# Kernel tuning notes

Hardware: AMD Instinct MI355X
Metric: run time of the kernel (lower is better)

Reference implementation:

```python
import jax, jax.numpy as jnp
import numpy as np

B, S, D = 2, 2048, 2048
NQ, NKV = 32, 8
HD = D // NQ  # 64
THETA = 10000.0


def _rope_tables(seq_len, head_dim, theta):
    k = jnp.arange(0, head_dim, 2)[: head_dim // 2].astype(jnp.float32)
    inv_freq = 1.0 / (theta ** (k / head_dim))
    pos = jnp.arange(seq_len, dtype=jnp.float32)
    ang = pos[:, None] * inv_freq[None, :]          # [S, HD/2]
    ang = jnp.concatenate([ang, ang], axis=-1)       # [S, HD]
    return jnp.cos(ang), jnp.sin(ang)


def _apply_rope(x, cos, sin):
    # x: [B, H, S, HD]; cos/sin: [S, HD]
    h = x.shape[-1] // 2
    x1, x2 = x[..., :h], x[..., h:]
    rotated = jnp.concatenate([-x2, x1], axis=-1)
    return (x * cos[None, None] + rotated * sin[None, None]).astype(x.dtype)


def setup_inputs() -> dict:
    key = jax.random.key(0)
    ks = jax.random.split(key, 6)
    x = jax.random.normal(ks[0], (B, S, D), dtype=jnp.float32)
    attention_mask = jnp.ones((B, S), dtype=jnp.int32)
    Wq = jax.random.normal(ks[1], (NQ * HD, D), dtype=jnp.float32) * 0.02
    Wk = jax.random.normal(ks[2], (NKV * HD, D), dtype=jnp.float32) * 0.02
    Wv = jax.random.normal(ks[3], (NKV * HD, D), dtype=jnp.float32) * 0.02
    Wo = jax.random.normal(ks[4], (D, D), dtype=jnp.float32) * 0.02
    return {"x": x, "attention_mask": attention_mask,
            "Wq": Wq, "Wk": Wk, "Wv": Wv, "Wo": Wo}


def reference(x, attention_mask, Wq, Wk, Wv, Wo):
    b, s, d = x.shape
    # projections (nn.Linear: y = x @ W.T)
    q = jnp.einsum('bsd,od->bso', x, Wq).reshape(b, s, NQ, HD).transpose(0, 2, 1, 3)
    k = jnp.einsum('bsd,od->bso', x, Wk).reshape(b, s, NKV, HD).transpose(0, 2, 1, 3)
    v = jnp.einsum('bsd,od->bso', x, Wv).reshape(b, s, NKV, HD).transpose(0, 2, 1, 3)
    cos, sin = _rope_tables(s, HD, THETA)
    q = _apply_rope(q, cos, sin)
    k = _apply_rope(k, cos, sin)
    g = NQ // NKV
    k = jnp.repeat(k, g, axis=1)  # [b, NQ, s, HD]
    v = jnp.repeat(v, g, axis=1)
    attn = jnp.einsum('bhqd,bhkd->bhqk', q, k)
    causal = jnp.triu(jnp.ones((s, s), dtype=bool), k=1)
    attn = jnp.where(causal[None, None], -jnp.inf, attn)
    attn = jax.nn.softmax(attn / jnp.sqrt(jnp.float32(HD)), axis=-1)
    out = jnp.einsum('bhqk,bhkd->bhqd', attn, v)
    out = out.transpose(0, 2, 1, 3).reshape(b, s, d)
    return jnp.einsum('bsd,od->bso', out, Wo)
```

## Files before the change

### kernel.cpp

```cpp
#include <hip/hip_runtime.h>

#define B_   2
#define S_   2048
#define D_   2048
#define NQ_  32
#define NKV_ 8
#define HD_  64

typedef unsigned short u16;
typedef __bf16 bf16x8 __attribute__((ext_vector_type(8)));
typedef __bf16 bf16x4 __attribute__((ext_vector_type(4)));
typedef short  s16x4  __attribute__((ext_vector_type(4)));
typedef float  f32x4  __attribute__((ext_vector_type(4)));

#define GLB __attribute__((address_space(1)))
#define LDS __attribute__((address_space(3)))

__device__ inline u16 f2b(float f){
  union { float f; unsigned u; } v; v.f = f;
  unsigned r = (v.u + 0x7fffu + ((v.u >> 16) & 1u)) >> 16;
  return (u16)r;
}

__device__ inline f32x4 mfma16(bf16x4 a, bf16x4 b, f32x4 c){
  union U { bf16x4 b; s16x4 s; };
  U ua, ub; ua.b = a; ub.b = b;
  return __builtin_amdgcn_mfma_f32_16x16x16bf16_1k(ua.s, ub.s, c, 0, 0, 0);
}

__global__ void k_f2b_all(const float* __restrict__ x,  const float* __restrict__ wq,
                          const float* __restrict__ wk, const float* __restrict__ wv,
                          const float* __restrict__ wo,
                          u16* __restrict__ xb, u16* __restrict__ wqkvb, u16* __restrict__ wob){
  int i = blockIdx.x * blockDim.x + threadIdx.x;
  const float* src; u16* dst; int off;
  if (i < 2097152)      { src = x;  dst = xb;                  off = i; }
  else if (i < 3145728) { src = wq; dst = wqkvb;               off = i - 2097152; }
  else if (i < 3407872) { src = wk; dst = wqkvb + 2048*2048;   off = i - 3145728; }
  else if (i < 3670016) { src = wv; dst = wqkvb + 2560*2048;   off = i - 3407872; }
  else                  { src = wo; dst = wob;                 off = i - 3670016; }
  float4 f = ((const float4*)src)[off];
  uint2 pk;
  pk.x = (unsigned)f2b(f.x) | ((unsigned)f2b(f.y) << 16);
  pk.y = (unsigned)f2b(f.z) | ((unsigned)f2b(f.w) << 16);
  ((uint2*)dst)[off] = pk;
}

#define GEMM_CORE(K)                                                           \
  __shared__ __align__(16) u16 As[128*64];                                     \
  __shared__ __align__(16) u16 Bs[128*64];                                     \
  const int tid  = threadIdx.x;                                               \
  const int lane = tid & 63;                                                  \
  const int wave = tid >> 6;                                                  \
  const int wm = wave >> 1, wn = wave & 1;                                    \
  const int quad = lane >> 4, l16 = lane & 15;                                \
  const u16* Ab = A  + (size_t)blockIdx.y * 128 * (K);                        \
  const u16* Bb = Bm + (size_t)blockIdx.x * 128 * (K);                        \
  f32x4 acc[4][4];                                                            \
  for (int i = 0; i < 4; i++)                                                 \
    for (int j = 0; j < 4; j++) acc[i][j] = (f32x4){0.f, 0.f, 0.f, 0.f};      \
  const int R0 = wave * 32;                                                   \
  const int lr = lane >> 3;                                                   \
  const int gc = ((lane & 7) ^ lr) * 8;                                       \
  const int sk = l16 & 7;                                                     \
  for (int k0 = 0; k0 < (K); k0 += 64){                                       \
    __syncthreads();                                                          \
    _Pragma("unroll")                                                         \
    for (int m = 0; m < 4; m++){                                              \
      const u16* ga = Ab + (size_t)(R0 + m*8 + lr) * (K) + k0 + gc;           \
      const u16* gb = Bb + (size_t)(R0 + m*8 + lr) * (K) + k0 + gc;           \
      __builtin_amdgcn_global_load_lds((const GLB void*)ga, (LDS void*)&As[(R0 + m*8)*64], 16, 0, 0); \
      __builtin_amdgcn_global_load_lds((const GLB void*)gb, (LDS void*)&Bs[(R0 + m*8)*64], 16, 0, 0); \
    }                                                                          \
    __syncthreads();                                                          \
    bf16x8 af[4][2], bfr[4][2];                                               \
    _Pragma("unroll")                                                         \
    for (int i = 0; i < 4; i++)                                               \
      _Pragma("unroll")                                                       \
      for (int h = 0; h < 2; h++)                                             \
        af[i][h]  = *(const bf16x8*)&As[(wm*64 + i*16 + l16)*64 + (((h*4 + quad) ^ sk)*8)]; \
    _Pragma("unroll")                                                         \
    for (int j = 0; j < 4; j++)                                               \
      _Pragma("unroll")                                                       \
      for (int h = 0; h < 2; h++)                                             \
        bfr[j][h] = *(const bf16x8*)&Bs[(wn*64 + j*16 + l16)*64 + (((h*4 + quad) ^ sk)*8)]; \
    _Pragma("unroll")                                                         \
    for (int i = 0; i < 4; i++)                                               \
      _Pragma("unroll")                                                       \
      for (int j = 0; j < 4; j++){                                            \
        acc[i][j] = __builtin_amdgcn_mfma_f32_16x16x32_bf16(af[i][0], bfr[j][0], acc[i][j], 0, 0, 0); \
        acc[i][j] = __builtin_amdgcn_mfma_f32_16x16x32_bf16(af[i][1], bfr[j][1], acc[i][j], 0, 0, 0); \
      }                                                                        \
  }

#define QSCALE 0.18033688011112042f
__global__ __launch_bounds__(256, 3) void k_gemm_qkv(const u16* __restrict__ A,
                                                     const u16* __restrict__ Bm,
                                                     u16* __restrict__ qT,
                                                     u16* __restrict__ kT,
                                                     u16* __restrict__ vT){
  GEMM_CORE(2048)

  const int cb = blockIdx.x*128 + wn*64;

  if (cb < 2560){
    const bool isq = (cb < 2048);
    const int hh   = (isq ? cb : (cb - 2048)) >> 6;
    const int NH   = isq ? NQ_ : NKV_;
    u16* base      = isq ? qT : kT;
    const float sc = isq ? QSCALE : 1.0f;
    #pragma unroll
    for (int j = 0; j < 2; j++){
      const int d2 = j*16 + l16;
      const float invf = __expf(-(float)d2 * (9.210340371976184f / 32.0f));
      #pragma unroll
      for (int i = 0; i < 4; i++){
        const int row0 = blockIdx.y*128 + wm*64 + i*16 + quad*4;
        #pragma unroll
        for (int r = 0; r < 4; r++){
          const int row = row0 + r;
          const int s = row & (S_ - 1), b = row >> 11;
          float ang = (float)s * invf;
          float sn = __sinf(ang), cs = __cosf(ang);
          const float x1 = acc[i][j][r] * sc, x2 = acc[i][j+2][r] * sc;
          u16* drow = base + ((size_t)(b*NH + hh) * S_ + s) * 64;
          drow[d2]      = f2b(x1*cs - x2*sn);
          drow[d2 + 32] = f2b(x2*cs + x1*sn);
        }
      }
    }
  } else {
    const int fbase = cb - 2560;
    #pragma unroll
    for (int j = 0; j < 4; j++){
      const int f = fbase + j*16 + l16;
      const int kvh = f >> 6, d = f & 63;
      #pragma unroll
      for (int i = 0; i < 4; i++){
        const int row0 = blockIdx.y*128 + wm*64 + i*16 + quad*4;
        const int s0 = row0 & (S_ - 1), b = row0 >> 11;
        uint2 pk;
        pk.x = (unsigned)f2b(acc[i][j][0]) | ((unsigned)f2b(acc[i][j][1]) << 16);
        pk.y = (unsigned)f2b(acc[i][j][2]) | ((unsigned)f2b(acc[i][j][3]) << 16);
        *(uint2*)(vT + ((size_t)(b*NKV_ + kvh) * 64 + d) * S_ + s0) = pk;
      }
    }
  }
}

__global__ __launch_bounds__(256, 3) void k_gemm_bt(const u16* __restrict__ A,
                                                    const u16* __restrict__ Bm,
                                                    float* __restrict__ C,
                                                    int N){
  GEMM_CORE(2048)
  for (int i = 0; i < 4; i++){
    int row0 = blockIdx.y*128 + wm*64 + i*16 + quad*4;
    for (int j = 0; j < 4; j++){
      int col = blockIdx.x*128 + wn*64 + j*16 + l16;
      for (int r = 0; r < 4; r++)
        C[(size_t)(row0 + r) * N + col] = acc[i][j][r];
    }
  }
}

__global__ __launch_bounds__(256) void k_attn(const u16* __restrict__ qT,
                                              const u16* __restrict__ kT,
                                              const u16* __restrict__ vT,
                                              u16* __restrict__ aout){
  __shared__ __align__(16) u16 Ks[2][64*64];
  __shared__ __align__(16) u16 Vs[2][64*64];

  const int bid  = blockIdx.x;
  const int tp   = bid & 7;
  const int h    = (bid >> 3) & 31;
  const int b    = bid >> 8;
  const int kvh  = h >> 2;
  const int lane = threadIdx.x & 63, w = threadIdx.x >> 6;
  const int quad = lane >> 4, l16 = lane & 15;

  const u16* Qh = qT + (size_t)(b*NQ_ + h)    * S_ * 64;
  const u16* Kh = kT + (size_t)(b*NKV_ + kvh) * S_ * 64;
  const u16* Vh = vT + (size_t)(b*NKV_ + kvh) * 64 * S_;

  const int rr = lane >> 3;
  const int gg = (lane & 7) ^ rr;
  const int R  = w * 16;

  auto stage = [&](int c, int buf){
    const int kb = c * 64;
    const u16* gk0 = Kh + (size_t)(kb + R + rr)     * 64 + gg*8;
    const u16* gk1 = Kh + (size_t)(kb + R + 8 + rr) * 64 + gg*8;
    const u16* gv0 = Vh + (size_t)(R + rr)     * S_ + kb + gg*8;
    const u16* gv1 = Vh + (size_t)(R + 8 + rr) * S_ + kb + gg*8;
    __builtin_amdgcn_global_load_lds((const GLB void*)gk0, (LDS void*)&Ks[buf][R*64],     16, 0, 0);
    __builtin_amdgcn_global_load_lds((const GLB void*)gk1, (LDS void*)&Ks[buf][(R+8)*64], 16, 0, 0);
    __builtin_amdgcn_global_load_lds((const GLB void*)gv0, (LDS void*)&Vs[buf][R*64],     16, 0, 0);
    __builtin_amdgcn_global_load_lds((const GLB void*)gv1, (LDS void*)&Vs[buf][(R+8)*64], 16, 0, 0);
  };

  const int sw = l16 & 7;

  for (int ph = 0; ph < 2; ph++){
    const int T   = ph ? (15 - tp) : tp;
    const int qb0 = 2*T, qb1 = 2*T + 1;
    const int qr0 = T*128 + w*16 + l16;
    const int qr1 = qr0 + 64;

    if (ph == 1) __syncthreads();
    stage(0, 0);

    bf16x8 qf[2][2];
    qf[0][0] = *(const bf16x8*)(Qh + (size_t)qr0*64 + quad*8);
    qf[0][1] = *(const bf16x8*)(Qh + (size_t)qr0*64 + 32 + quad*8);
    qf[1][0] = *(const bf16x8*)(Qh + (size_t)qr1*64 + quad*8);
    qf[1][1] = *(const bf16x8*)(Qh + (size_t)qr1*64 + 32 + quad*8);

    f32x4 o[2][4];
    #pragma unroll
    for (int s = 0; s < 2; s++)
      for (int dt = 0; dt < 4; dt++) o[s][dt] = (f32x4){0.f, 0.f, 0.f, 0.f};
    float lrow[2] = {0.f, 0.f};

    for (int c = 0; c <= qb1; c++){
      const int buf = c & 1;
      __syncthreads();
      if (c < qb1) stage(c+1, buf^1);

      const bool act0  = (c <= qb0);
      const bool diag0 = (c == qb0);
      const bool diag1 = (c == qb1);

      bf16x4 pk[2][4];
      #pragma unroll
      for (int t = 0; t < 4; t++){
        const bool n0 = act0 && !(diag0 && t > w);
        const bool n1 = !(diag1 && t > w);
        if (!n0 && !n1) continue;
        const int row = t*16 + l16;
        bf16x8 ka0 = *(const bf16x8*)&Ks[buf][row*64 + (((quad    ) ^ sw)*8)];
        bf16x8 ka1 = *(const bf16x8*)&Ks[buf][row*64 + (((quad + 4) ^ sw)*8)];
        #pragma unroll
        for (int s = 0; s < 2; s++){
          if (s == 0 ? !n0 : !n1) continue;
          f32x4 z = (f32x4){0.f, 0.f, 0.f, 0.f};
          z = __builtin_amdgcn_mfma_f32_16x16x32_bf16(ka0, qf[s][0], z, 0, 0, 0);
          z = __builtin_amdgcn_mfma_f32_16x16x32_bf16(ka1, qf[s][1], z, 0, 0, 0);
          if ((s == 0 ? diag0 : diag1) && t == w){
            #pragma unroll
            for (int r = 0; r < 4; r++)
              if (quad*4 + r > l16) z[r] = -1e30f;
          }
          #pragma unroll
          for (int r = 0; r < 4; r++){
            float p = exp2f(z[r]);
            lrow[s] += p;
            pk[s][t][r] = (__bf16)p;
          }
        }
      }

      #pragma unroll
      for (int dt = 0; dt < 4; dt++){
        const int row = dt*16 + l16;
        #pragma unroll
        for (int t = 0; t < 4; t++){
          const bool n0 = act0 && !(diag0 && t > w);
          const bool n1 = !(diag1 && t > w);
          if (!n0 && !n1) continue;
          const int ch = (2*t + (quad >> 1)) ^ sw;
          bf16x4 va = *(const bf16x4*)&Vs[buf][row*64 + ch*8 + (quad & 1)*4];
          if (n0) o[0][dt] = mfma16(va, pk[0][t], o[0][dt]);
          if (n1) o[1][dt] = mfma16(va, pk[1][t], o[1][dt]);
        }
      }
    }

    #pragma unroll
    for (int s = 0; s < 2; s++){
      float lsum = lrow[s];
      lsum += __shfl_xor(lsum, 16, 64);
      lsum += __shfl_xor(lsum, 32, 64);
      float inv = 1.0f / lsum;
      const int qrow = s ? qr1 : qr0;
      u16* orow = aout + (size_t)(b*S_ + qrow) * D_ + h*64;
      #pragma unroll
      for (int dt = 0; dt < 4; dt++){
        uint2 pkd;
        u16 e0 = f2b(o[s][dt][0] * inv), e1 = f2b(o[s][dt][1] * inv);
        u16 e2 = f2b(o[s][dt][2] * inv), e3 = f2b(o[s][dt][3] * inv);
        pkd.x = (unsigned)e0 | ((unsigned)e1 << 16);
        pkd.y = (unsigned)e2 | ((unsigned)e3 << 16);
        *(uint2*)(orow + dt*16 + quad*4) = pkd;
      }
    }
  }
}

extern "C" void kernel_launch(void* const* d_in, const int* in_sizes, int n_in,
                              void* d_out, int out_size, void* d_ws, size_t ws_size,
                              hipStream_t stream){
  const float* x  = (const float*)d_in[0];
  const float* Wq = (const float*)d_in[2];
  const float* Wk = (const float*)d_in[3];
  const float* Wv = (const float*)d_in[4];
  const float* Wo = (const float*)d_in[5];

  char* ws = (char*)d_ws;
  u16* xb    = (u16*)(ws);
  u16* wqkvb = (u16*)(ws + 16777216);
  u16* wob   = (u16*)(ws + 29360128);
  u16* qTp   = (u16*)(ws + 37748736);
  u16* kTp   = (u16*)(ws + 54525952);
  u16* vTp   = (u16*)(ws + 58720256);
  u16* attnOut = xb;

  k_f2b_all<<<dim3(18432), 256, 0, stream>>>(x, Wq, Wk, Wv, Wo, xb, wqkvb, wob);

  k_gemm_qkv<<<dim3(24, 32), 256, 0, stream>>>(xb, wqkvb, qTp, kTp, vTp);

  k_attn<<<dim3(512), 256, 0, stream>>>(qTp, kTp, vTp, attnOut);

  k_gemm_bt<<<dim3(16, 32), 256, 0, stream>>>(attnOut, wob, (float*)d_out, 2048);
}
```

Before: 301.4 us.

## Split attention blocks per query tile, heavy-first order, cheaper exp and bf16 pack

The attention grid goes from 512 blocks, each handling a balanced pair of query tiles (T and 15-T), to 1024 blocks that each handle one 128-row tile. Tiles are scheduled largest-first, and the index order places the 8 KV heads and both batches in adjacent blocks, which may help K/V cache locality and load balance. The inner loop also switches to the hardware exp2 builtin, packs P to bf16 by truncation instead of rounding, and hoists the swizzle offsets. Truncating P loses a little precision, and single-tile blocks redo per-block setup and Q loads.

New measurement: 297.4 us. Within noise of the previous version (-1.3%).

```diff
diff --git a/kernel.cpp b/kernel.cpp
--- a/kernel.cpp
+++ b/kernel.cpp
@@ -26,6 +26,15 @@
   union U { bf16x4 b; s16x4 s; };
   U ua, ub; ua.b = a; ub.b = b;
   return __builtin_amdgcn_mfma_f32_16x16x16bf16_1k(ua.s, ub.s, c, 0, 0, 0);
+}
+
+__device__ inline bf16x4 pack4(float p0, float p1, float p2, float p3){
+  union { float f; unsigned u; } a, b, c, d;
+  a.f = p0; b.f = p1; c.f = p2; d.f = p3;
+  union { uint2 u; bf16x4 v; } r;
+  r.u.x = (a.u >> 16) | (b.u & 0xffff0000u);
+  r.u.y = (c.u >> 16) | (d.u & 0xffff0000u);
+  return r.v;
 }
 
 __global__ void k_f2b_all(const float* __restrict__ x,  const float* __restrict__ wq,
@@ -170,11 +179,12 @@
   __shared__ __align__(16) u16 Ks[2][64*64];
   __shared__ __align__(16) u16 Vs[2][64*64];
 
-  const int bid  = blockIdx.x;
-  const int tp   = bid & 7;
-  const int h    = (bid >> 3) & 31;
-  const int b    = bid >> 8;
-  const int kvh  = h >> 2;
+  const int bid = blockIdx.x;
+  const int kvh = bid & 7;
+  const int b   = (bid >> 3) & 1;
+  const int hq  = (bid >> 4) & 3;
+  const int T   = 15 - (bid >> 6);
+  const int h   = kvh*4 + hq;
   const int lane = threadIdx.x & 63, w = threadIdx.x >> 6;
   const int quad = lane >> 4, l16 = lane & 15;
 
@@ -198,100 +208,103 @@
     __builtin_amdgcn_global_load_lds((const GLB void*)gv1, (LDS void*)&Vs[buf][(R+8)*64], 16, 0, 0);
   };
 
-  const int sw = l16 & 7;
-
-  for (int ph = 0; ph < 2; ph++){
-    const int T   = ph ? (15 - tp) : tp;
-    const int qb0 = 2*T, qb1 = 2*T + 1;
-    const int qr0 = T*128 + w*16 + l16;
-    const int qr1 = qr0 + 64;
-
-    if (ph == 1) __syncthreads();
-    stage(0, 0);
-
-    bf16x8 qf[2][2];
-    qf[0][0] = *(const bf16x8*)(Qh + (size_t)qr0*64 + quad*8);
-    qf[0][1] = *(const bf16x8*)(Qh + (size_t)qr0*64 + 32 + quad*8);
-    qf[1][0] = *(const bf16x8*)(Qh + (size_t)qr1*64 + quad*8);
-    qf[1][1] = *(const bf16x8*)(Qh + (size_t)qr1*64 + 32 + quad*8);
-
-    f32x4 o[2][4];
-    #pragma unroll
-    for (int s = 0; s < 2; s++)
-      for (int dt = 0; dt < 4; dt++) o[s][dt] = (f32x4){0.f, 0.f, 0.f, 0.f};
-    float lrow[2] = {0.f, 0.f};
-
-    for (int c = 0; c <= qb1; c++){
-      const int buf = c & 1;
-      __syncthreads();
-      if (c < qb1) stage(c+1, buf^1);
-
-      const bool act0  = (c <= qb0);
-      const bool diag0 = (c == qb0);
-      const bool diag1 = (c == qb1);
-
-      bf16x4 pk[2][4];
+  const int sw    = l16 & 7;
+  const int koff0 = ((quad    ) ^ sw) * 8;
+  const int koff1 = ((quad + 4) ^ sw) * 8;
+  int voff[4];
+  #pragma unroll
+  for (int t = 0; t < 4; t++)
+    voff[t] = (((2*t + (quad >> 1)) ^ sw) * 8) + (quad & 1)*4;
+
+  const int qb0 = 2*T, qb1 = 2*T + 1;
+  const int qr0 = T*128 + w*16 + l16;
+  const int qr1 = qr0 + 64;
+
+  stage(0, 0);
+
+  bf16x8 qf[2][2];
+  qf[0][0] = *(const bf16x8*)(Qh + (size_t)qr0*64 + quad*8);
+  qf[0][1] = *(const bf16x8*)(Qh + (size_t)qr0*64 + 32 + quad*8);
+  qf[1][0] = *(const bf16x8*)(Qh + (size_t)qr1*64 + quad*8);
+  qf[1][1] = *(const bf16x8*)(Qh + (size_t)qr1*64 + 32 + quad*8);
+
+  f32x4 o[2][4];
+  #pragma unroll
+  for (int s = 0; s < 2; s++)
+    for (int dt = 0; dt < 4; dt++) o[s][dt] = (f32x4){0.f, 0.f, 0.f, 0.f};
+  float lrow[2] = {0.f, 0.f};
+
+  for (int c = 0; c <= qb1; c++){
+    const int buf = c & 1;
+    __syncthreads();
+    if (c < qb1) stage(c+1, buf^1);
+
+    const bool act0  = (c <= qb0);
+    const bool diag0 = (c == qb0);
+    const bool diag1 = (c == qb1);
+    const u16* Kb = &Ks[buf][0];
+    const u16* Vb = &Vs[buf][0];
+
+    bf16x4 pk[2][4];
+    #pragma unroll
+    for (int t = 0; t < 4; t++){
+      const bool n0 = act0 && !(diag0 && t > w);
+      const bool n1 = !(diag1 && t > w);
+      if (!n0 && !n1) continue;
+      const int rowb = (t*16 + l16)*64;
+      bf16x8 ka0 = *(const bf16x8*)&Kb[rowb + koff0];
+      bf16x8 ka1 = *(const bf16x8*)&Kb[rowb + koff1];
+      #pragma unroll
+      for (int s = 0; s < 2; s++){
+        if (s == 0 ? !n0 : !n1) continue;
+        f32x4 z = (f32x4){0.f, 0.f, 0.f, 0.f};
+        z = __builtin_amdgcn_mfma_f32_16x16x32_bf16(ka0, qf[s][0], z, 0, 0, 0);
+        z = __builtin_amdgcn_mfma_f32_16x16x32_bf16(ka1, qf[s][1], z, 0, 0, 0);
+        if ((s == 0 ? diag0 : diag1) && t == w){
+          #pragma unroll
+          for (int r = 0; r < 4; r++)
+            if (quad*4 + r > l16) z[r] = -1e30f;
+        }
+        float p0 = __builtin_amdgcn_exp2f(z[0]);
+        float p1 = __builtin_amdgcn_exp2f(z[1]);
+        float p2 = __builtin_amdgcn_exp2f(z[2]);
+        float p3 = __builtin_amdgcn_exp2f(z[3]);
+        lrow[s] += (p0 + p1) + (p2 + p3);
+        pk[s][t] = pack4(p0, p1, p2, p3);
+      }
+    }
+
+    #pragma unroll
+    for (int dt = 0; dt < 4; dt++){
+      const int rowb = (dt*16 + l16)*64;
       #pragma unroll
       for (int t = 0; t < 4; t++){
         const bool n0 = act0 && !(diag0 && t > w);
         const bool n1 = !(diag1 && t > w);
         if (!n0 && !n1) continue;
-        const int row = t*16 + l16;
-        bf16x8 ka0 = *(const bf16x8*)&Ks[buf][row*64 + (((quad    ) ^ sw)*8)];
-        bf16x8 ka1 = *(const bf16x8*)&Ks[buf][row*64 + (((quad + 4) ^ sw)*8)];
-        #pragma unroll
-        for (int s = 0; s < 2; s++){
-          if (s == 0 ? !n0 : !n1) continue;
-          f32x4 z = (f32x4){0.f, 0.f, 0.f, 0.f};
-          z = __builtin_amdgcn_mfma_f32_16x16x32_bf16(ka0, qf[s][0], z, 0, 0, 0);
-          z = __builtin_amdgcn_mfma_f32_16x16x32_bf16(ka1, qf[s][1], z, 0, 0, 0);
-          if ((s == 0 ? diag0 : diag1) && t == w){
-            #pragma unroll
-            for (int r = 0; r < 4; r++)
-              if (quad*4 + r > l16) z[r] = -1e30f;
-          }
-          #pragma unroll
-          for (int r = 0; r < 4; r++){
-            float p = exp2f(z[r]);
-            lrow[s] += p;
-            pk[s][t][r] = (__bf16)p;
-          }
-        }
+        bf16x4 va = *(const bf16x4*)&Vb[rowb + voff[t]];
+        if (n0) o[0][dt] = mfma16(va, pk[0][t], o[0][dt]);
+        if (n1) o[1][dt] = mfma16(va, pk[1][t], o[1][dt]);
       }
-
-      #pragma unroll
-      for (int dt = 0; dt < 4; dt++){
-        const int row = dt*16 + l16;
-        #pragma unroll
-        for (int t = 0; t < 4; t++){
-          const bool n0 = act0 && !(diag0 && t > w);
-          const bool n1 = !(diag1 && t > w);
-          if (!n0 && !n1) continue;
-          const int ch = (2*t + (quad >> 1)) ^ sw;
-          bf16x4 va = *(const bf16x4*)&Vs[buf][row*64 + ch*8 + (quad & 1)*4];
-          if (n0) o[0][dt] = mfma16(va, pk[0][t], o[0][dt]);
-          if (n1) o[1][dt] = mfma16(va, pk[1][t], o[1][dt]);
-        }
-      }
-    }
-
-    #pragma unroll
-    for (int s = 0; s < 2; s++){
-      float lsum = lrow[s];
-      lsum += __shfl_xor(lsum, 16, 64);
-      lsum += __shfl_xor(lsum, 32, 64);
-      float inv = 1.0f / lsum;
-      const int qrow = s ? qr1 : qr0;
-      u16* orow = aout + (size_t)(b*S_ + qrow) * D_ + h*64;
-      #pragma unroll
-      for (int dt = 0; dt < 4; dt++){
-        uint2 pkd;
-        u16 e0 = f2b(o[s][dt][0] * inv), e1 = f2b(o[s][dt][1] * inv);
-        u16 e2 = f2b(o[s][dt][2] * inv), e3 = f2b(o[s][dt][3] * inv);
-        pkd.x = (unsigned)e0 | ((unsigned)e1 << 16);
-        pkd.y = (unsigned)e2 | ((unsigned)e3 << 16);
-        *(uint2*)(orow + dt*16 + quad*4) = pkd;
-      }
+    }
+  }
+
+  #pragma unroll
+  for (int s = 0; s < 2; s++){
+    float lsum = lrow[s];
+    lsum += __shfl_xor(lsum, 16, 64);
+    lsum += __shfl_xor(lsum, 32, 64);
+    float inv = 1.0f / lsum;
+    const int qrow = s ? qr1 : qr0;
+    u16* orow = aout + (size_t)(b*S_ + qrow) * D_ + h*64;
+    #pragma unroll
+    for (int dt = 0; dt < 4; dt++){
+      uint2 pkd;
+      u16 e0 = f2b(o[s][dt][0] * inv), e1 = f2b(o[s][dt][1] * inv);
+      u16 e2 = f2b(o[s][dt][2] * inv), e3 = f2b(o[s][dt][3] * inv);
+      pkd.x = (unsigned)e0 | ((unsigned)e1 << 16);
+      pkd.y = (unsigned)e2 | ((unsigned)e3 << 16);
+      *(uint2*)(orow + dt*16 + quad*4) = pkd;
     }
   }
 }
@@ -318,7 +331,7 @@
 
   k_gemm_qkv<<<dim3(24, 32), 256, 0, stream>>>(xb, wqkvb, qTp, kTp, vTp);
 
-  k_attn<<<dim3(512), 256, 0, stream>>>(qTp, kTp, vTp, attnOut);
+  k_attn<<<dim3(1024), 256, 0, stream>>>(qTp, kTp, vTp, attnOut);
 
   k_gemm_bt<<<dim3(16, 32), 256, 0, stream>>>(attnOut, wob, (float*)d_out, 2048);
 }
```
